# Optimization experiments

Measured on AMD Instinct MI355X. Metric: run time of the kernel, lower is better.

Reference implementation:

```python
import jax, jax.numpy as jnp
import numpy as np

B, S, E, H = 2, 2048, 1024, 16
D = E // H  # head dim = 64


def setup_inputs() -> dict:
    key = jax.random.key(0)
    ks = jax.random.split(key, 8)
    return {
        "query": jax.random.normal(ks[0], (B, S, E), dtype=jnp.float32),
        "key": jax.random.normal(ks[1], (B, S, E), dtype=jnp.float32),
        "value": jax.random.normal(ks[2], (B, S, E), dtype=jnp.float32),
        "qkv_weight": jax.random.normal(ks[3], (3 * E, E), dtype=jnp.float32) * 0.02,
        "qkv_bias": jax.random.normal(ks[4], (3 * E,), dtype=jnp.float32) * 0.02,
        "proj_weight": jax.random.normal(ks[5], (E, E), dtype=jnp.float32) * 0.02,
        "proj_bias": jax.random.normal(ks[6], (E,), dtype=jnp.float32) * 0.02,
        "mask": jax.random.normal(ks[7], (S, S), dtype=jnp.float32),
    }


def reference(query, key, value, qkv_weight, qkv_bias, proj_weight, proj_bias, mask):
    # Split fused QKV weight/bias into per-projection chunks ([E,E] each).
    wq, wk, wv = jnp.split(qkv_weight, 3, axis=0)
    bq, bk, bv = jnp.split(qkv_bias, 3, axis=0)

    def proj_heads(x, w, b):
        # [B,S,E] @ [E,E]^T + [E] -> [B,H,S,D]
        y = jnp.einsum("bse,fe->bsf", x, w) + b
        return y.reshape(B, S, H, D).transpose(0, 2, 1, 3)

    q = proj_heads(query, wq, bq)
    k = proj_heads(key, wk, bk)
    v = proj_heads(value, wv, bv)

    scale = 1.0 / jnp.sqrt(jnp.asarray(D, dtype=q.dtype))
    # scores: [B,H,S,S]; mask_type 0 -> additive [S,S] float mask broadcast over B,H
    scores = jnp.einsum("bhsd,bhtd->bhst", q, k) * scale + mask[None, None, :, :]
    attn = jax.nn.softmax(scores, axis=-1)
    ctx = jnp.einsum("bhst,bhtd->bhsd", attn, v)  # [B,H,S,D]
    ctx = ctx.transpose(0, 2, 1, 3).reshape(B, S, E)
    # output projection
    return jnp.einsum("bse,fe->bsf", ctx, proj_weight) + proj_bias
```

## Files before the change

kernel.cpp:

```cpp
#include <hip/hip_runtime.h>
#include <hip/hip_bf16.h>

typedef unsigned short u16;
typedef __attribute__((ext_vector_type(8))) __bf16 bf16x8;
typedef __attribute__((ext_vector_type(4))) __bf16 bf16x4;
typedef __attribute__((ext_vector_type(4))) float f32x4;

#define LOG2E 1.44269504f

#if __has_builtin(__builtin_amdgcn_exp2f)
#define EXP2F(x) __builtin_amdgcn_exp2f(x)
#else
#define EXP2F(x) __expf((x) * 0.69314718f)
#endif

#define GLL16(gptr, lptr) \
  __builtin_amdgcn_global_load_lds((__attribute__((address_space(1))) void*)(gptr), \
                                   (__attribute__((address_space(3))) void*)(lptr), 16, 0, 0)

static __device__ __forceinline__ u16 f2bf(float f) {
  union { float f; unsigned u; } v; v.f = f;
  unsigned r = (v.u + 0x7FFFu + ((v.u >> 16) & 1u)) >> 16;
  return (u16)r;
}

__global__ __launch_bounds__(256) void cvt_all(
    const float* __restrict__ q, const float* __restrict__ k, const float* __restrict__ v,
    const float* __restrict__ w1, const float* __restrict__ w2,
    u16* __restrict__ xq, u16* __restrict__ xk, u16* __restrict__ xv,
    u16* __restrict__ wq, u16* __restrict__ wp) {
  const int b = blockIdx.x;
  const float* src; u16* dst; int off;
  if (b < 4096)       { src = q;  dst = xq; off = b; }
  else if (b < 8192)  { src = k;  dst = xk; off = b - 4096; }
  else if (b < 12288) { src = v;  dst = xv; off = b - 8192; }
  else if (b < 15360) { src = w1; dst = wq; off = b - 12288; }
  else                { src = w2; dst = wp; off = b - 15360; }
  const int i = off * 256 + threadIdx.x;
  float4 vv = ((const float4*)src)[i];
  ushort4 o;
  o.x = f2bf(vv.x); o.y = f2bf(vv.y); o.z = f2bf(vv.z); o.w = f2bf(vv.w);
  ((ushort4*)dst)[i] = o;
}

__global__ __launch_bounds__(256, 2) void qkv_gemm(
    const u16* __restrict__ xq, const u16* __restrict__ xk, const u16* __restrict__ xv,
    const u16* __restrict__ wbf, const float* __restrict__ bias,
    u16* __restrict__ qout, u16* __restrict__ kout, u16* __restrict__ vtout) {
  __shared__ u16 Al[128 * 32];
  __shared__ u16 Bl[128 * 32];
  const int tid = threadIdx.x;
  const int lane = tid & 63;
  const int w = tid >> 6;
  const int wr = w >> 1, wc = w & 1;
  const int nb = blockIdx.x, mb = blockIdx.y;
  const int row0 = mb * 128;
  const int ncol0 = nb * 128;
  const int which = nb >> 3;
  const u16* A = (which == 0) ? xq : (which == 1) ? xk : xv;
  const u16* Bw = wbf + (size_t)ncol0 * 1024;

  f32x4 acc[4][4];
  f32x4 zero = {0.f, 0.f, 0.f, 0.f};
#pragma unroll
  for (int i = 0; i < 4; i++)
#pragma unroll
    for (int j = 0; j < 4; j++) acc[i][j] = zero;

  const int srow = w * 16 + (lane >> 2);
  const int scol = (lane & 3) * 8;

  for (int k0 = 0; k0 < 1024; k0 += 32) {
#pragma unroll
    for (int p = 0; p < 2; p++) {
      const u16* ga = A + (size_t)(row0 + p * 64 + srow) * 1024 + k0 + scol;
      GLL16(ga, &Al[(p * 64 + w * 16) * 32]);
      const u16* gb = Bw + (size_t)(p * 64 + srow) * 1024 + k0 + scol;
      GLL16(gb, &Bl[(p * 64 + w * 16) * 32]);
    }
    __syncthreads();
    bf16x8 af[4], bfr[4];
#pragma unroll
    for (int mi = 0; mi < 4; mi++)
      af[mi] = *(const bf16x8*)&Al[(wr * 64 + mi * 16 + (lane & 15)) * 32 + (lane >> 4) * 8];
#pragma unroll
    for (int ni = 0; ni < 4; ni++)
      bfr[ni] = *(const bf16x8*)&Bl[(wc * 64 + ni * 16 + (lane & 15)) * 32 + (lane >> 4) * 8];
#pragma unroll
    for (int mi = 0; mi < 4; mi++)
#pragma unroll
      for (int ni = 0; ni < 4; ni++)
        acc[mi][ni] = __builtin_amdgcn_mfma_f32_16x16x32_bf16(af[mi], bfr[ni], acc[mi][ni], 0, 0, 0);
    __syncthreads();
  }

#pragma unroll
  for (int mi = 0; mi < 4; mi++) {
    const int rb = row0 + wr * 64 + mi * 16 + (lane >> 4) * 4;
#pragma unroll
    for (int ni = 0; ni < 4; ni++) {
      const int c = ncol0 + wc * 64 + ni * 16 + (lane & 15);
      const float bs = bias[c];
      const float sc = (which == 0) ? (0.125f * LOG2E) : 1.0f;
      const int fm = c & 1023;
      const int h = fm >> 6, d = fm & 63;
#pragma unroll
      for (int r = 0; r < 4; r++) {
        const int rr = rb + r;
        const int b = rr >> 11, s = rr & 2047;
        const u16 val = f2bf((acc[mi][ni][r] + bs) * sc);
        if (which == 0)
          qout[(((size_t)(b * 16 + h)) * 2048 + s) * 64 + d] = val;
        else if (which == 1)
          kout[(((size_t)(b * 16 + h)) * 2048 + s) * 64 + d] = val;
        else
          vtout[(((size_t)(b * 16 + h)) * 64 + d) * 2048 + s] = val;
      }
    }
  }
}


#define STAGE_KV(KOFF, VOFF)                                        \
  *(float4*)(ldsb + (KOFF) + S0) = kr0;                             \
  *(float2*)(ldsb + (VOFF) + VS0a) = make_float2(vr0.x, vr0.y);     \
  *(float2*)(ldsb + (VOFF) + VS0b) = make_float2(vr0.z, vr0.w);

#define ATTN_TILE(PAR, MC)                                                         \
  {                                                                                \
    f32x4 s0_, s1_, s2_, s3_;                                                      \
    __builtin_amdgcn_s_setprio(1);                                                 \
    {                                                                              \
      bf16x8 a_, b_;                                                               \
      a_ = *(const bf16x8*)(ldsb + Kr0 + 0 + (PAR));                               \
      b_ = *(const bf16x8*)(ldsb + Kr1 + 0 + (PAR));                               \
      s0_ = __builtin_amdgcn_mfma_f32_16x16x32_bf16(a_, q0, MC[0], 0, 0, 0);       \
      s0_ = __builtin_amdgcn_mfma_f32_16x16x32_bf16(b_, q1, s0_, 0, 0, 0);         \
      a_ = *(const bf16x8*)(ldsb + Kr0 + 2048 + (PAR));                            \
      b_ = *(const bf16x8*)(ldsb + Kr1 + 2048 + (PAR));                            \
      s1_ = __builtin_amdgcn_mfma_f32_16x16x32_bf16(a_, q0, MC[1], 0, 0, 0);       \
      s1_ = __builtin_amdgcn_mfma_f32_16x16x32_bf16(b_, q1, s1_, 0, 0, 0);         \
      a_ = *(const bf16x8*)(ldsb + Kr0 + 4096 + (PAR));                            \
      b_ = *(const bf16x8*)(ldsb + Kr1 + 4096 + (PAR));                            \
      s2_ = __builtin_amdgcn_mfma_f32_16x16x32_bf16(a_, q0, MC[2], 0, 0, 0);       \
      s2_ = __builtin_amdgcn_mfma_f32_16x16x32_bf16(b_, q1, s2_, 0, 0, 0);         \
      a_ = *(const bf16x8*)(ldsb + Kr0 + 6144 + (PAR));                            \
      b_ = *(const bf16x8*)(ldsb + Kr1 + 6144 + (PAR));                            \
      s3_ = __builtin_amdgcn_mfma_f32_16x16x32_bf16(a_, q0, MC[3], 0, 0, 0);       \
      s3_ = __builtin_amdgcn_mfma_f32_16x16x32_bf16(b_, q1, s3_, 0, 0, 0);         \
    }                                                                              \
    __builtin_amdgcn_s_setprio(0);                                                 \
    float pm = fmaxf(fmaxf(fmaxf(fmaxf(s0_[0], s0_[1]), fmaxf(s0_[2], s0_[3])),    \
                           fmaxf(fmaxf(s1_[0], s1_[1]), fmaxf(s1_[2], s1_[3]))),   \
                     fmaxf(fmaxf(fmaxf(s2_[0], s2_[1]), fmaxf(s2_[2], s2_[3])),    \
                           fmaxf(fmaxf(s3_[0], s3_[1]), fmaxf(s3_[2], s3_[3]))));  \
                     \
    s0_[0] = EXP2F(s0_[0] - m); s0_[1] = EXP2F(s0_[1] - m);                        \
    s0_[2] = EXP2F(s0_[2] - m); s0_[3] = EXP2F(s0_[3] - m);                        \
    s1_[0] = EXP2F(s1_[0] - m); s1_[1] = EXP2F(s1_[1] - m);                        \
    s1_[2] = EXP2F(s1_[2] - m); s1_[3] = EXP2F(s1_[3] - m);                        \
    s2_[0] = EXP2F(s2_[0] - m); s2_[1] = EXP2F(s2_[1] - m);                        \
    s2_[2] = EXP2F(s2_[2] - m); s2_[3] = EXP2F(s2_[3] - m);                        \
    s3_[0] = EXP2F(s3_[0] - m); s3_[1] = EXP2F(s3_[1] - m);                        \
    s3_[2] = EXP2F(s3_[2] - m); s3_[3] = EXP2F(s3_[3] - m);                        \
    float ps = ((s0_[0] + s0_[1]) + (s0_[2] + s0_[3])) +                           \
               ((s1_[0] + s1_[1]) + (s1_[2] + s1_[3])) +                           \
               ((s2_[0] + s2_[1]) + (s2_[2] + s2_[3])) +                           \
               ((s3_[0] + s3_[1]) + (s3_[2] + s3_[3]));                            \
    pm = fmaxf(pm, __shfl_xor(pm, 16));                                            \
    pm = fmaxf(pm, __shfl_xor(pm, 32));                                            \
    if (__any(pm > m + 8.0f)) {                 \
      const float mn = fmaxf(m, pm);                                               \
      const float al = EXP2F(m - mn);                                              \
      m = mn; lsum *= al; ps *= al;                                                \
      s0_ *= al; s1_ *= al; s2_ *= al; s3_ *= al;                                  \
      ctx[0] *= al; ctx[1] *= al; ctx[2] *= al; ctx[3] *= al;                      \
    }                                                                              \
    lsum += ps;                                                                    \
           \
    bf16x8 pa0, pa1;                                                               \
    pa0[0] = (__bf16)s0_[0]; pa0[1] = (__bf16)s0_[1];                              \
    pa0[2] = (__bf16)s0_[2]; pa0[3] = (__bf16)s0_[3];                              \
    pa0[4] = (__bf16)s1_[0]; pa0[5] = (__bf16)s1_[1];                              \
    pa0[6] = (__bf16)s1_[2]; pa0[7] = (__bf16)s1_[3];                              \
    pa1[0] = (__bf16)s2_[0]; pa1[1] = (__bf16)s2_[1];                              \
    pa1[2] = (__bf16)s2_[2]; pa1[3] = (__bf16)s2_[3];                              \
    pa1[4] = (__bf16)s3_[0]; pa1[5] = (__bf16)s3_[1];                              \
    pa1[6] = (__bf16)s3_[2]; pa1[7] = (__bf16)s3_[3];                              \
    {                                                                              \
      bf16x8 v00 = *(const bf16x8*)(ldsb + Kr0 + 16384 + (PAR));                   \
      bf16x8 v01 = *(const bf16x8*)(ldsb + Kr1 + 16384 + (PAR));                   \
      bf16x8 v10 = *(const bf16x8*)(ldsb + Kr0 + 18432 + (PAR));                   \
      bf16x8 v11 = *(const bf16x8*)(ldsb + Kr1 + 18432 + (PAR));                   \
      bf16x8 v20 = *(const bf16x8*)(ldsb + Kr0 + 20480 + (PAR));                   \
      bf16x8 v21 = *(const bf16x8*)(ldsb + Kr1 + 20480 + (PAR));                   \
      bf16x8 v30 = *(const bf16x8*)(ldsb + Kr0 + 22528 + (PAR));                   \
      bf16x8 v31 = *(const bf16x8*)(ldsb + Kr1 + 22528 + (PAR));                   \
      __builtin_amdgcn_s_setprio(1);                                               \
      ctx[0] = __builtin_amdgcn_mfma_f32_16x16x32_bf16(v00, pa0, ctx[0], 0, 0, 0); \
      ctx[0] = __builtin_amdgcn_mfma_f32_16x16x32_bf16(v01, pa1, ctx[0], 0, 0, 0); \
      ctx[1] = __builtin_amdgcn_mfma_f32_16x16x32_bf16(v10, pa0, ctx[1], 0, 0, 0); \
      ctx[1] = __builtin_amdgcn_mfma_f32_16x16x32_bf16(v11, pa1, ctx[1], 0, 0, 0); \
      ctx[2] = __builtin_amdgcn_mfma_f32_16x16x32_bf16(v20, pa0, ctx[2], 0, 0, 0); \
      ctx[2] = __builtin_amdgcn_mfma_f32_16x16x32_bf16(v21, pa1, ctx[2], 0, 0, 0); \
      ctx[3] = __builtin_amdgcn_mfma_f32_16x16x32_bf16(v30, pa0, ctx[3], 0, 0, 0); \
      ctx[3] = __builtin_amdgcn_mfma_f32_16x16x32_bf16(v31, pa1, ctx[3], 0, 0, 0); \
      __builtin_amdgcn_s_setprio(0);                                               \
    }                                                                              \
  }

__global__ __launch_bounds__(512, 4) void attn_fwd(
    const u16* __restrict__ qbf, const u16* __restrict__ kbf, const u16* __restrict__ vtbf,
    const float* __restrict__ mask, u16* __restrict__ ctxout) {
  __shared__ u16 lds[16384];
  char* ldsb = (char*)lds;
  const int tid = threadIdx.x, lane = tid & 63, w = tid >> 6;
  const int qL = lane & 15, g = lane >> 4;
  const int x = (qL & 7) << 4;
  const int bh = blockIdx.x, qt = blockIdx.y;
  const int qbase = qt * 128;
  const size_t hbase = (size_t)bh * 2048 * 64;
  const int qrow = qbase + w * 16 + qL;

  const int Kr0 = qL * 128 + ((g * 16) ^ x);
  const int Kr1 = qL * 128 + ((g * 16 + 64) ^ x);
  const int srow = tid >> 3;
  const int scol = (tid & 7) * 8;
  const int S0 = srow * 128 + (((tid & 7) * 16) ^ ((srow & 7) << 4));
  const int a_ = tid & 7;
  const int vW1 = ((a_ >> 2) << 6) + (((2 * a_) & 3) << 4) + (((a_ >> 1) & 1) << 3);
  const int vW2 = ((a_ >> 2) << 6) + (((2 * a_ + 1) & 3) << 4) + (((a_ >> 1) & 1) << 3);
  const int sxr = (srow & 7) << 4;
  const int VS0a = srow * 128 + (vW1 ^ sxr);
  const int VS0b = srow * 128 + (vW2 ^ sxr);

  bf16x8 q0 = *(const bf16x8*)&qbf[hbase + (size_t)qrow * 64 + g * 8];
  bf16x8 q1 = *(const bf16x8*)&qbf[hbase + (size_t)qrow * 64 + 32 + g * 8];

  float4 kr0, vr0;
  kr0 = *(const float4*)&kbf[hbase + (size_t)srow * 64 + scol];
  vr0 = *(const float4*)&vtbf[hbase + (size_t)srow * 2048 + scol];
  STAGE_KV(0, 16384)
  kr0 = *(const float4*)&kbf[hbase + (size_t)(64 + srow) * 64 + scol];
  vr0 = *(const float4*)&vtbf[hbase + (size_t)srow * 2048 + 64 + scol];

  const u16* kp = kbf + hbase + (size_t)(128 + srow) * 64 + scol;
  const u16* vp = vtbf + hbase + (size_t)srow * 2048 + 128 + scol;
  const float* mp = mask + (size_t)qrow * 2048 + g * 4;

  f32x4 mA[4], mB[4];
#pragma unroll
  for (int tb = 0; tb < 4; tb++)
    mA[tb] = (*(const f32x4*)(mp + tb * 16)) * LOG2E;

  float m = 0.f, lsum = 0.f;
  f32x4 ctx[4];
  f32x4 zero = {0.f, 0.f, 0.f, 0.f};
#pragma unroll
  for (int db = 0; db < 4; db++) ctx[db] = zero;

  __syncthreads();

  for (int i = 0; i < 16; ++i) {
    STAGE_KV(8192, 24576)
    if (i < 15) {
      kr0 = *(const float4*)kp;
      vr0 = *(const float4*)vp;
      kp += 4096; vp += 64;
    }
#pragma unroll
    for (int tb = 0; tb < 4; tb++)
      mB[tb] = (*(const f32x4*)(mp + 64 + tb * 16)) * LOG2E;
    ATTN_TILE(0, mA)
    __syncthreads();

    if (i < 15) {
      STAGE_KV(0, 16384)
      kr0 = *(const float4*)kp;
      vr0 = *(const float4*)vp;
      kp += 4096; vp += 64;
#pragma unroll
      for (int tb = 0; tb < 4; tb++)
        mA[tb] = (*(const f32x4*)(mp + 128 + tb * 16)) * LOG2E;
    }
    ATTN_TILE(8192, mB)
    mp += 128;
    __syncthreads();
  }

  lsum += __shfl_xor(lsum, 16);
  lsum += __shfl_xor(lsum, 32);
  const float inv = 1.0f / lsum;
  const int b = bh >> 4, h = bh & 15;
  u16* orow = ctxout + (size_t)(b * 2048 + qrow) * 1024 + h * 64;
#pragma unroll
  for (int db = 0; db < 4; db++) {
    bf16x4 o;
    o[0] = (__bf16)(ctx[db][0] * inv);
    o[1] = (__bf16)(ctx[db][1] * inv);
    o[2] = (__bf16)(ctx[db][2] * inv);
    o[3] = (__bf16)(ctx[db][3] * inv);
    *(bf16x4*)&orow[db * 16 + g * 4] = o;
  }
}

__global__ __launch_bounds__(256, 2) void proj_gemm(
    const u16* __restrict__ ctx, const u16* __restrict__ wbf,
    const float* __restrict__ bias, float* __restrict__ out) {
  __shared__ u16 Al[128 * 32];
  __shared__ u16 Bl[128 * 32];
  const int tid = threadIdx.x;
  const int lane = tid & 63;
  const int w = tid >> 6;
  const int wr = w >> 1, wc = w & 1;
  const int nb = blockIdx.x, mb = blockIdx.y;
  const int row0 = mb * 128;
  const int ncol0 = nb * 128;
  const u16* Bw = wbf + (size_t)ncol0 * 1024;

  f32x4 acc[4][4];
  f32x4 zero = {0.f, 0.f, 0.f, 0.f};
#pragma unroll
  for (int i = 0; i < 4; i++)
#pragma unroll
    for (int j = 0; j < 4; j++) acc[i][j] = zero;

  const int srow = w * 16 + (lane >> 2);
  const int scol = (lane & 3) * 8;

  for (int k0 = 0; k0 < 1024; k0 += 32) {
#pragma unroll
    for (int p = 0; p < 2; p++) {
      const u16* ga = ctx + (size_t)(row0 + p * 64 + srow) * 1024 + k0 + scol;
      GLL16(ga, &Al[(p * 64 + w * 16) * 32]);
      const u16* gb = Bw + (size_t)(p * 64 + srow) * 1024 + k0 + scol;
      GLL16(gb, &Bl[(p * 64 + w * 16) * 32]);
    }
    __syncthreads();
    bf16x8 af[4], bfr[4];
#pragma unroll
    for (int mi = 0; mi < 4; mi++)
      af[mi] = *(const bf16x8*)&Al[(wr * 64 + mi * 16 + (lane & 15)) * 32 + (lane >> 4) * 8];
#pragma unroll
    for (int ni = 0; ni < 4; ni++)
      bfr[ni] = *(const bf16x8*)&Bl[(wc * 64 + ni * 16 + (lane & 15)) * 32 + (lane >> 4) * 8];
#pragma unroll
    for (int mi = 0; mi < 4; mi++)
#pragma unroll
      for (int ni = 0; ni < 4; ni++)
        acc[mi][ni] = __builtin_amdgcn_mfma_f32_16x16x32_bf16(af[mi], bfr[ni], acc[mi][ni], 0, 0, 0);
    __syncthreads();
  }

#pragma unroll
  for (int mi = 0; mi < 4; mi++) {
    const int rb = row0 + wr * 64 + mi * 16 + (lane >> 4) * 4;
#pragma unroll
    for (int ni = 0; ni < 4; ni++) {
      const int c = ncol0 + wc * 64 + ni * 16 + (lane & 15);
      const float bs = bias[c];
#pragma unroll
      for (int r = 0; r < 4; r++)
        out[(size_t)(rb + r) * 1024 + c] = acc[mi][ni][r] + bs;
    }
  }
}

extern "C" void kernel_launch(void* const* d_in, const int* in_sizes, int n_in,
                              void* d_out, int out_size, void* d_ws, size_t ws_size,
                              hipStream_t stream) {
  const float* query = (const float*)d_in[0];
  const float* key   = (const float*)d_in[1];
  const float* value = (const float*)d_in[2];
  const float* qkvw  = (const float*)d_in[3];
  const float* qkvb  = (const float*)d_in[4];
  const float* projw = (const float*)d_in[5];
  const float* projb = (const float*)d_in[6];
  const float* mask  = (const float*)d_in[7];

  char* ws = (char*)d_ws;
  u16* xq    = (u16*)(ws + 0);
  u16* xk    = (u16*)(ws + 8388608);
  u16* xv    = (u16*)(ws + 16777216);
  u16* wqkv  = (u16*)(ws + 25165824);
  u16* wproj = (u16*)(ws + 31457280);
  u16* qb    = (u16*)(ws + 33554432);
  u16* kb    = (u16*)(ws + 41943040);
  u16* vt    = (u16*)(ws + 50331648);
  u16* cx    = xq;

  cvt_all<<<16384, 256, 0, stream>>>(query, key, value, qkvw, projw, xq, xk, xv, wqkv, wproj);
  qkv_gemm<<<dim3(24, 32), 256, 0, stream>>>(xq, xk, xv, wqkv, qkvb, qb, kb, vt);
  attn_fwd<<<dim3(32, 16), 512, 0, stream>>>(qb, kb, vt, mask, cx);
  proj_gemm<<<dim3(8, 32), 256, 0, stream>>>(cx, wproj, projb, (float*)d_out);
}
```

Measured before the change: 160.9 us.

## Split attention over two key halves and merge partials in a combine kernel

The attention kernel gains a third grid dimension that splits the 2048 keys into two halves, so twice as many blocks run, each doing half the loop iterations. Each block writes its unnormalized partial context in bf16, plus its running max and sum, into reused workspace regions. A new combine kernel rescales and merges the two partials with the log-sum-exp weights and writes the final context for the output projection. The aim is to fill more of the GPU during attention, at the cost of an extra launch, extra memory traffic and bf16 rounding of unnormalized partials.

Measured after the change: 170.9 us. +6.2%, slower.

```diff
diff --git a/kernel.cpp b/kernel.cpp
--- a/kernel.cpp
+++ b/kernel.cpp
@@ -211,13 +211,14 @@
 
 __global__ __launch_bounds__(512, 4) void attn_fwd(
     const u16* __restrict__ qbf, const u16* __restrict__ kbf, const u16* __restrict__ vtbf,
-    const float* __restrict__ mask, u16* __restrict__ ctxout) {
+    const float* __restrict__ mask, u16* __restrict__ pctx, float2* __restrict__ mlbuf) {
   __shared__ u16 lds[16384];
   char* ldsb = (char*)lds;
   const int tid = threadIdx.x, lane = tid & 63, w = tid >> 6;
   const int qL = lane & 15, g = lane >> 4;
   const int x = (qL & 7) << 4;
-  const int bh = blockIdx.x, qt = blockIdx.y;
+  const int bh = blockIdx.x, qt = blockIdx.y, z = blockIdx.z;
+  const int th = z << 10;
   const int qbase = qt * 128;
   const size_t hbase = (size_t)bh * 2048 * 64;
   const int qrow = qbase + w * 16 + qL;
@@ -238,15 +239,15 @@
   bf16x8 q1 = *(const bf16x8*)&qbf[hbase + (size_t)qrow * 64 + 32 + g * 8];
 
   float4 kr0, vr0;
-  kr0 = *(const float4*)&kbf[hbase + (size_t)srow * 64 + scol];
-  vr0 = *(const float4*)&vtbf[hbase + (size_t)srow * 2048 + scol];
+  kr0 = *(const float4*)&kbf[hbase + (size_t)(th + srow) * 64 + scol];
+  vr0 = *(const float4*)&vtbf[hbase + (size_t)srow * 2048 + th + scol];
   STAGE_KV(0, 16384)
-  kr0 = *(const float4*)&kbf[hbase + (size_t)(64 + srow) * 64 + scol];
-  vr0 = *(const float4*)&vtbf[hbase + (size_t)srow * 2048 + 64 + scol];
-
-  const u16* kp = kbf + hbase + (size_t)(128 + srow) * 64 + scol;
-  const u16* vp = vtbf + hbase + (size_t)srow * 2048 + 128 + scol;
-  const float* mp = mask + (size_t)qrow * 2048 + g * 4;
+  kr0 = *(const float4*)&kbf[hbase + (size_t)(th + 64 + srow) * 64 + scol];
+  vr0 = *(const float4*)&vtbf[hbase + (size_t)srow * 2048 + th + 64 + scol];
+
+  const u16* kp = kbf + hbase + (size_t)(th + 128 + srow) * 64 + scol;
+  const u16* vp = vtbf + hbase + (size_t)srow * 2048 + th + 128 + scol;
+  const float* mp = mask + (size_t)qrow * 2048 + th + g * 4;
 
   f32x4 mA[4], mB[4];
 #pragma unroll
@@ -261,9 +262,9 @@
 
   __syncthreads();
 
-  for (int i = 0; i < 16; ++i) {
+  for (int i = 0; i < 8; ++i) {
     STAGE_KV(8192, 24576)
-    if (i < 15) {
+    if (i < 7) {
       kr0 = *(const float4*)kp;
       vr0 = *(const float4*)vp;
       kp += 4096; vp += 64;
@@ -274,7 +275,7 @@
     ATTN_TILE(0, mA)
     __syncthreads();
 
-    if (i < 15) {
+    if (i < 7) {
       STAGE_KV(0, 16384)
       kr0 = *(const float4*)kp;
       vr0 = *(const float4*)vp;
@@ -290,17 +291,48 @@
 
   lsum += __shfl_xor(lsum, 16);
   lsum += __shfl_xor(lsum, 32);
-  const float inv = 1.0f / lsum;
-  const int b = bh >> 4, h = bh & 15;
-  u16* orow = ctxout + (size_t)(b * 2048 + qrow) * 1024 + h * 64;
+  const int qlocal = w * 16 + qL;
+  const size_t pidx = ((size_t)(z * 512 + bh * 16 + qt) * 128 + qlocal);
+  u16* prow = pctx + pidx * 64;
 #pragma unroll
   for (int db = 0; db < 4; db++) {
     bf16x4 o;
-    o[0] = (__bf16)(ctx[db][0] * inv);
-    o[1] = (__bf16)(ctx[db][1] * inv);
-    o[2] = (__bf16)(ctx[db][2] * inv);
-    o[3] = (__bf16)(ctx[db][3] * inv);
-    *(bf16x4*)&orow[db * 16 + g * 4] = o;
+    o[0] = (__bf16)ctx[db][0];
+    o[1] = (__bf16)ctx[db][1];
+    o[2] = (__bf16)ctx[db][2];
+    o[3] = (__bf16)ctx[db][3];
+    *(bf16x4*)&prow[db * 16 + g * 4] = o;
+  }
+  if (g == 0) mlbuf[pidx] = make_float2(m, lsum);
+}
+
+__global__ __launch_bounds__(256) void attn_combine(
+    const u16* __restrict__ pctx, const float2* __restrict__ mlbuf,
+    u16* __restrict__ cx) {
+  const int blk = blockIdx.x;
+  const int bh = blk >> 4, qt = blk & 15;
+  const int t = threadIdx.x;
+  const int q = t >> 1, dz = (t & 1) * 32;
+  const size_t i0 = (size_t)blk * 128 + q;
+  const size_t i1 = (size_t)(512 + blk) * 128 + q;
+  const float2 ml0 = mlbuf[i0], ml1 = mlbuf[i1];
+  const float mm = fmaxf(ml0.x, ml1.x);
+  const float fa = EXP2F(ml0.x - mm), fb = EXP2F(ml1.x - mm);
+  const float inv = 1.0f / (ml0.y * fa + ml1.y * fb);
+  const float wa = fa * inv, wb = fb * inv;
+  const u16* p0 = pctx + i0 * 64 + dz;
+  const u16* p1 = pctx + i1 * 64 + dz;
+  const int b = bh >> 4, h = bh & 15;
+  u16* orow = cx + (size_t)(b * 2048 + qt * 128 + q) * 1024 + h * 64 + dz;
+#pragma unroll
+  for (int c = 0; c < 4; c++) {
+    bf16x8 c0 = *(const bf16x8*)&p0[c * 8];
+    bf16x8 c1 = *(const bf16x8*)&p1[c * 8];
+    bf16x8 o;
+#pragma unroll
+    for (int e = 0; e < 8; e++)
+      o[e] = (__bf16)((float)c0[e] * wa + (float)c1[e] * wb);
+    *(bf16x8*)&orow[c * 8] = o;
   }
 }
 
@@ -388,9 +420,12 @@
   u16* kb    = (u16*)(ws + 41943040);
   u16* vt    = (u16*)(ws + 50331648);
   u16* cx    = xq;
+  u16* pctx  = xk;
+  float2* mlbuf = (float2*)(ws + 25165824);
 
   cvt_all<<<16384, 256, 0, stream>>>(query, key, value, qkvw, projw, xq, xk, xv, wqkv, wproj);
   qkv_gemm<<<dim3(24, 32), 256, 0, stream>>>(xq, xk, xv, wqkv, qkvb, qb, kb, vt);
-  attn_fwd<<<dim3(32, 16), 512, 0, stream>>>(qb, kb, vt, mask, cx);
+  attn_fwd<<<dim3(32, 16, 2), 512, 0, stream>>>(qb, kb, vt, mask, pctx, mlbuf);
+  attn_combine<<<512, 256, 0, stream>>>(pctx, mlbuf, cx);
   proj_gemm<<<dim3(8, 32), 256, 0, stream>>>(cx, wproj, projb, (float*)d_out);
 }
```
